# Optimization experiments

Hardware: AMD Instinct MI355X
Metric: run time of the kernel (lower is better)

The kernel has to match this reference:

```python
import jax, jax.numpy as jnp
import numpy as np

N_CLUSTERS = 256
EMBED_DIM = 128
ALPHA = 1.0


def setup_inputs() -> dict:
    key = jax.random.key(0)
    k1, k2 = jax.random.split(key)
    inputs = jax.random.normal(k1, (200000, EMBED_DIM), dtype=jnp.float32)
    clusters = jax.random.normal(k2, (N_CLUSTERS, EMBED_DIM), dtype=jnp.float32)
    return {"inputs": inputs, "clusters": clusters}


def reference(inputs, clusters):
    # Squared euclidean distance via the GEMM trick instead of an [N, K, D]
    x_sq = jnp.sum(inputs * inputs, axis=1, keepdims=True)          # [N, 1]
    c_sq = jnp.sum(clusters * clusters, axis=1)[None, :]             # [1, K]
    cross = inputs @ clusters.T                                      # [N, K]
    dist2 = jnp.maximum(x_sq + c_sq - 2.0 * cross, 0.0)              # [N, K]
    q = 1.0 / (1.0 + dist2 / ALPHA)
    q = q ** ((ALPHA + 1.0) / 2.0)
    q = q / jnp.sum(q, axis=1, keepdims=True)
    return q
```

## Files before the change

### kernel.cpp

```cpp
#include <hip/hip_runtime.h>


#define DIM 128
#define NK  256
#define TM  64
#define THREADS 512
#define LSTR 136

typedef __attribute__((ext_vector_type(8))) short short8;
typedef __attribute__((ext_vector_type(4))) float floatx4;

__device__ __forceinline__ unsigned short bf16_rne(float f) {
    unsigned int u = __float_as_uint(f);
    return (unsigned short)((u + 0x7fffu + ((u >> 16) & 1u)) >> 16);
}
__device__ __forceinline__ float bf16_f(unsigned short h) {
    return __uint_as_float(((unsigned int)h) << 16);
}

__global__ __launch_bounds__(THREADS, 4) void cluster_q_mfma(
    const float* __restrict__ x,
    const float* __restrict__ c,
    float* __restrict__ out)
{
    __shared__ __align__(16) unsigned short xs_hi[TM][LSTR];
    __shared__ __align__(16) unsigned short xs_lo[TM][LSTR];
    __shared__ float xsq_s[TM];
    __shared__ float psum[TM][8];
    __shared__ float inv_s[TM];

    const int tid  = threadIdx.x;
    const int wave = tid >> 6;
    const int lane = tid & 63;
    const int lm   = lane & 15;
    const int q4   = lane >> 4;
    const size_t row0 = (size_t)blockIdx.x * TM;

    {
        const int r  = tid >> 3;
        const int cb = (tid & 7) * 16;
        const float4* xg = (const float4*)(x + (row0 + r) * DIM + cb);
        float4 f4[4];
        #pragma unroll
        for (int i = 0; i < 4; ++i) f4[i] = xg[i];
        const float* fv = (const float*)f4;
        union { unsigned short u[16]; short8 v[2]; } H, L;
        float s = 0.f;
        #pragma unroll
        for (int i = 0; i < 16; ++i) {
            float f = fv[i];
            s = fmaf(f, f, s);
            unsigned short h = bf16_rne(f);
            H.u[i] = h;
            L.u[i] = bf16_rne(f - bf16_f(h));
        }
        *(short8*)&xs_hi[r][cb]     = H.v[0];
        *(short8*)&xs_hi[r][cb + 8] = H.v[1];
        *(short8*)&xs_lo[r][cb]     = L.v[0];
        *(short8*)&xs_lo[r][cb + 8] = L.v[1];
        s += __shfl_xor(s, 1);
        s += __shfl_xor(s, 2);
        s += __shfl_xor(s, 4);
        if ((tid & 7) == 0) xsq_s[r] = s;
    }

    short8 bf[2][4];
    float csq[2];
    #pragma unroll
    for (int ct = 0; ct < 2; ++ct) {
        float cp = 0.f;
        const int col = wave * 32 + ct * 16 + lm;
        #pragma unroll
        for (int ks = 0; ks < 4; ++ks) {
            const float4* cg = (const float4*)(c + col * DIM + ks * 32 + q4 * 8);
            float4 b0 = cg[0], b1 = cg[1];
            const float* bv0 = (const float*)&b0;
            const float* bv1 = (const float*)&b1;
            union { unsigned short u[8]; short8 v; } B;
            #pragma unroll
            for (int i = 0; i < 4; ++i) {
                float f = bv0[i];
                cp = fmaf(f, f, cp);
                B.u[i] = bf16_rne(f);
            }
            #pragma unroll
            for (int i = 0; i < 4; ++i) {
                float f = bv1[i];
                cp = fmaf(f, f, cp);
                B.u[4 + i] = bf16_rne(f);
            }
            bf[ct][ks] = B.v;
        }
        cp += __shfl_xor(cp, 16);
        cp += __shfl_xor(cp, 32);
        csq[ct] = cp;
    }

    floatx4 acc[4][2];
    #pragma unroll
    for (int rt = 0; rt < 4; ++rt)
        #pragma unroll
        for (int ct = 0; ct < 2; ++ct)
            acc[rt][ct] = (floatx4){0.f, 0.f, 0.f, 0.f};

    __syncthreads();

    #pragma unroll
    for (int ks = 0; ks < 4; ++ks) {
        const int ko = ks * 32 + q4 * 8;
        #pragma unroll
        for (int rt = 0; rt < 4; ++rt) {
            short8 ah = *(const short8*)&xs_hi[rt * 16 + lm][ko];
            short8 al = *(const short8*)&xs_lo[rt * 16 + lm][ko];
            #pragma unroll
            for (int ct = 0; ct < 2; ++ct) {
                acc[rt][ct] = __builtin_amdgcn_mfma_f32_16x16x32_bf16(ah, bf[ct][ks], acc[rt][ct], 0, 0, 0);
                acc[rt][ct] = __builtin_amdgcn_mfma_f32_16x16x32_bf16(al, bf[ct][ks], acc[rt][ct], 0, 0, 0);
            }
        }
    }

    #pragma unroll
    for (int rt = 0; rt < 4; ++rt) {
        #pragma unroll
        for (int reg = 0; reg < 4; ++reg) {
            const int r = rt * 16 + q4 * 4 + reg;
            const float xq = xsq_s[r];
            float p = 0.f;
            #pragma unroll
            for (int ct = 0; ct < 2; ++ct) {
                float d2 = xq + csq[ct] - 2.f * acc[rt][ct][reg];
                d2 = fmaxf(d2, 0.f);
                float q = 1.f / (1.f + d2);
                acc[rt][ct][reg] = q;
                p += q;
            }
            p += __shfl_xor(p, 1);
            p += __shfl_xor(p, 2);
            p += __shfl_xor(p, 4);
            p += __shfl_xor(p, 8);
            if (lm == 0) psum[r][wave] = p;
        }
    }
    __syncthreads();

    if (tid < TM) {
        float s = 0.f;
        #pragma unroll
        for (int w = 0; w < 8; ++w) s += psum[tid][w];
        inv_s[tid] = 1.f / s;
    }
    __syncthreads();

    #pragma unroll
    for (int rt = 0; rt < 4; ++rt) {
        #pragma unroll
        for (int reg = 0; reg < 4; ++reg) {
            const int r = rt * 16 + q4 * 4 + reg;
            const float inv = inv_s[r];
            #pragma unroll
            for (int ct = 0; ct < 2; ++ct) {
                out[(row0 + r) * NK + wave * 32 + ct * 16 + lm] = acc[rt][ct][reg] * inv;
            }
        }
    }
}

extern "C" void kernel_launch(void* const* d_in, const int* in_sizes, int n_in,
                              void* d_out, int out_size, void* d_ws, size_t ws_size,
                              hipStream_t stream) {
    const float* x = (const float*)d_in[0];
    const float* c = (const float*)d_in[1];
    float* out = (float*)d_out;
    int N = in_sizes[0] / DIM;
    cluster_q_mfma<<<dim3(N / TM), dim3(THREADS), 0, stream>>>(x, c, out);
}
```

Before: 329.1 us.

## Precompute bf16 clusters in prep kernel and give each wave full rows

Adds a small prep kernel that converts the cluster matrix to bf16 in MFMA fragment order and computes cluster squared norms into workspace, so the main kernel stops redoing that work in every block. The main kernel now uses 256 threads, with each wave owning 16 rows across all 256 clusters and loading x straight into registers. This removes the x LDS staging, the cross-wave partial-sum exchange and two barriers. It also uses fast reciprocal intrinsics. The cost is a second launch, reading B fragments from global/L2 in each block, and more accumulator registers per thread.

```diff
diff --git a/kernel.cpp b/kernel.cpp
--- a/kernel.cpp
+++ b/kernel.cpp
@@ -3,9 +3,6 @@
 
 #define DIM 128
 #define NK  256
-#define TM  64
-#define THREADS 512
-#define LSTR 136
 
 typedef __attribute__((ext_vector_type(8))) short short8;
 typedef __attribute__((ext_vector_type(4))) float floatx4;
@@ -18,151 +15,141 @@
     return __uint_as_float(((unsigned int)h) << 16);
 }
 
-__global__ __launch_bounds__(THREADS, 4) void cluster_q_mfma(
+__global__ void prep_clusters(const float* __restrict__ c,
+                              unsigned short* __restrict__ wb,
+                              float* __restrict__ wcsq)
+{
+    if (blockIdx.x < 8) {
+        const int gid  = blockIdx.x * 512 + threadIdx.x;
+        const int lane = gid & 63;
+        const int ks   = (gid >> 6) & 3;
+        const int ct   = gid >> 8;
+        const int lm   = lane & 15;
+        const int q4   = lane >> 4;
+        const int col  = ct * 16 + lm;
+        const float4* cg = (const float4*)(c + col * DIM + ks * 32 + q4 * 8);
+        float4 v0 = cg[0], v1 = cg[1];
+        const float* f0 = (const float*)&v0;
+        const float* f1 = (const float*)&v1;
+        union { unsigned short u[8]; short8 v; } B;
+        #pragma unroll
+        for (int i = 0; i < 4; ++i) B.u[i] = bf16_rne(f0[i]);
+        #pragma unroll
+        for (int i = 0; i < 4; ++i) B.u[4 + i] = bf16_rne(f1[i]);
+        ((short8*)wb)[gid] = B.v;
+    } else {
+        const int t = threadIdx.x;
+        const int col = t >> 1, half = t & 1;
+        const float4* cg = (const float4*)(c + col * DIM + half * 64);
+        float s = 0.f;
+        #pragma unroll
+        for (int i = 0; i < 16; ++i) {
+            float4 v = cg[i];
+            s = fmaf(v.x, v.x, s); s = fmaf(v.y, v.y, s);
+            s = fmaf(v.z, v.z, s); s = fmaf(v.w, v.w, s);
+        }
+        s += __shfl_xor(s, 1);
+        if (!half) wcsq[col] = s;
+    }
+}
+
+__global__ __launch_bounds__(256, 3) void cluster_q_v2(
     const float* __restrict__ x,
-    const float* __restrict__ c,
+    const unsigned short* __restrict__ wb,
+    const float* __restrict__ wcsq,
     float* __restrict__ out)
 {
-    __shared__ __align__(16) unsigned short xs_hi[TM][LSTR];
-    __shared__ __align__(16) unsigned short xs_lo[TM][LSTR];
-    __shared__ float xsq_s[TM];
-    __shared__ float psum[TM][8];
-    __shared__ float inv_s[TM];
+    __shared__ float csq_s[NK];
+    const int tid  = threadIdx.x;
+    csq_s[tid] = wcsq[tid];
 
-    const int tid  = threadIdx.x;
     const int wave = tid >> 6;
     const int lane = tid & 63;
     const int lm   = lane & 15;
     const int q4   = lane >> 4;
-    const size_t row0 = (size_t)blockIdx.x * TM;
+    const size_t row0 = (size_t)blockIdx.x * 64 + wave * 16;
 
-    {
-        const int r  = tid >> 3;
-        const int cb = (tid & 7) * 16;
-        const float4* xg = (const float4*)(x + (row0 + r) * DIM + cb);
-        float4 f4[4];
+    short8 ah[4], al[4];
+    float xq = 0.f;
+    const float* xrow = x + (row0 + lm) * DIM;
+    #pragma unroll
+    for (int ks = 0; ks < 4; ++ks) {
+        const float4* xg = (const float4*)(xrow + ks * 32 + q4 * 8);
+        float4 v0 = xg[0], v1 = xg[1];
+        const float* f0 = (const float*)&v0;
+        const float* f1 = (const float*)&v1;
+        union { unsigned short u[8]; short8 v; } H, L;
         #pragma unroll
-        for (int i = 0; i < 4; ++i) f4[i] = xg[i];
-        const float* fv = (const float*)f4;
-        union { unsigned short u[16]; short8 v[2]; } H, L;
-        float s = 0.f;
-        #pragma unroll
-        for (int i = 0; i < 16; ++i) {
-            float f = fv[i];
-            s = fmaf(f, f, s);
+        for (int i = 0; i < 4; ++i) {
+            float f = f0[i];
+            xq = fmaf(f, f, xq);
             unsigned short h = bf16_rne(f);
             H.u[i] = h;
             L.u[i] = bf16_rne(f - bf16_f(h));
         }
-        *(short8*)&xs_hi[r][cb]     = H.v[0];
-        *(short8*)&xs_hi[r][cb + 8] = H.v[1];
-        *(short8*)&xs_lo[r][cb]     = L.v[0];
-        *(short8*)&xs_lo[r][cb + 8] = L.v[1];
-        s += __shfl_xor(s, 1);
-        s += __shfl_xor(s, 2);
-        s += __shfl_xor(s, 4);
-        if ((tid & 7) == 0) xsq_s[r] = s;
+        #pragma unroll
+        for (int i = 0; i < 4; ++i) {
+            float f = f1[i];
+            xq = fmaf(f, f, xq);
+            unsigned short h = bf16_rne(f);
+            H.u[4 + i] = h;
+            L.u[4 + i] = bf16_rne(f - bf16_f(h));
+        }
+        ah[ks] = H.v;
+        al[ks] = L.v;
     }
+    xq += __shfl_xor(xq, 16);
+    xq += __shfl_xor(xq, 32);
 
-    short8 bf[2][4];
-    float csq[2];
+    floatx4 acc[16];
     #pragma unroll
-    for (int ct = 0; ct < 2; ++ct) {
-        float cp = 0.f;
-        const int col = wave * 32 + ct * 16 + lm;
+    for (int ct = 0; ct < 16; ++ct) {
+        const short8* bp = (const short8*)wb + (ct * 256 + lane);
+        floatx4 a = (floatx4){0.f, 0.f, 0.f, 0.f};
         #pragma unroll
         for (int ks = 0; ks < 4; ++ks) {
-            const float4* cg = (const float4*)(c + col * DIM + ks * 32 + q4 * 8);
-            float4 b0 = cg[0], b1 = cg[1];
-            const float* bv0 = (const float*)&b0;
-            const float* bv1 = (const float*)&b1;
-            union { unsigned short u[8]; short8 v; } B;
-            #pragma unroll
-            for (int i = 0; i < 4; ++i) {
-                float f = bv0[i];
-                cp = fmaf(f, f, cp);
-                B.u[i] = bf16_rne(f);
-            }
-            #pragma unroll
-            for (int i = 0; i < 4; ++i) {
-                float f = bv1[i];
-                cp = fmaf(f, f, cp);
-                B.u[4 + i] = bf16_rne(f);
-            }
-            bf[ct][ks] = B.v;
+            short8 b = bp[ks * 64];
+            a = __builtin_amdgcn_mfma_f32_16x16x32_bf16(ah[ks], b, a, 0, 0, 0);
+            a = __builtin_amdgcn_mfma_f32_16x16x32_bf16(al[ks], b, a, 0, 0, 0);
         }
-        cp += __shfl_xor(cp, 16);
-        cp += __shfl_xor(cp, 32);
-        csq[ct] = cp;
+        acc[ct] = a;
     }
-
-    floatx4 acc[4][2];
-    #pragma unroll
-    for (int rt = 0; rt < 4; ++rt)
-        #pragma unroll
-        for (int ct = 0; ct < 2; ++ct)
-            acc[rt][ct] = (floatx4){0.f, 0.f, 0.f, 0.f};
 
     __syncthreads();
 
+    float xs4[4];
     #pragma unroll
-    for (int ks = 0; ks < 4; ++ks) {
-        const int ko = ks * 32 + q4 * 8;
+    for (int r = 0; r < 4; ++r) xs4[r] = __shfl(xq, q4 * 4 + r);
+
+    float rsum[4] = {0.f, 0.f, 0.f, 0.f};
+    #pragma unroll
+    for (int ct = 0; ct < 16; ++ct) {
+        const float cq = csq_s[ct * 16 + lm];
         #pragma unroll
-        for (int rt = 0; rt < 4; ++rt) {
-            short8 ah = *(const short8*)&xs_hi[rt * 16 + lm][ko];
-            short8 al = *(const short8*)&xs_lo[rt * 16 + lm][ko];
-            #pragma unroll
-            for (int ct = 0; ct < 2; ++ct) {
-                acc[rt][ct] = __builtin_amdgcn_mfma_f32_16x16x32_bf16(ah, bf[ct][ks], acc[rt][ct], 0, 0, 0);
-                acc[rt][ct] = __builtin_amdgcn_mfma_f32_16x16x32_bf16(al, bf[ct][ks], acc[rt][ct], 0, 0, 0);
-            }
+        for (int r = 0; r < 4; ++r) {
+            float d2 = fmaf(-2.f, acc[ct][r], xs4[r] + cq);
+            d2 = fmaxf(d2, 0.f);
+            float q = __builtin_amdgcn_rcpf(1.f + d2);
+            acc[ct][r] = q;
+            rsum[r] += q;
         }
+    }
+    #pragma unroll
+    for (int r = 0; r < 4; ++r) {
+        rsum[r] += __shfl_xor(rsum[r], 1);
+        rsum[r] += __shfl_xor(rsum[r], 2);
+        rsum[r] += __shfl_xor(rsum[r], 4);
+        rsum[r] += __shfl_xor(rsum[r], 8);
+        rsum[r] = __builtin_amdgcn_rcpf(rsum[r]);
     }
 
     #pragma unroll
-    for (int rt = 0; rt < 4; ++rt) {
+    for (int r = 0; r < 4; ++r) {
+        float* op = out + (row0 + q4 * 4 + r) * NK + lm;
+        const float inv = rsum[r];
         #pragma unroll
-        for (int reg = 0; reg < 4; ++reg) {
-            const int r = rt * 16 + q4 * 4 + reg;
-            const float xq = xsq_s[r];
-            float p = 0.f;
-            #pragma unroll
-            for (int ct = 0; ct < 2; ++ct) {
-                float d2 = xq + csq[ct] - 2.f * acc[rt][ct][reg];
-                d2 = fmaxf(d2, 0.f);
-                float q = 1.f / (1.f + d2);
-                acc[rt][ct][reg] = q;
-                p += q;
-            }
-            p += __shfl_xor(p, 1);
-            p += __shfl_xor(p, 2);
-            p += __shfl_xor(p, 4);
-            p += __shfl_xor(p, 8);
-            if (lm == 0) psum[r][wave] = p;
-        }
-    }
-    __syncthreads();
-
-    if (tid < TM) {
-        float s = 0.f;
-        #pragma unroll
-        for (int w = 0; w < 8; ++w) s += psum[tid][w];
-        inv_s[tid] = 1.f / s;
-    }
-    __syncthreads();
-
-    #pragma unroll
-    for (int rt = 0; rt < 4; ++rt) {
-        #pragma unroll
-        for (int reg = 0; reg < 4; ++reg) {
-            const int r = rt * 16 + q4 * 4 + reg;
-            const float inv = inv_s[r];
-            #pragma unroll
-            for (int ct = 0; ct < 2; ++ct) {
-                out[(row0 + r) * NK + wave * 32 + ct * 16 + lm] = acc[rt][ct][reg] * inv;
-            }
-        }
+        for (int ct = 0; ct < 16; ++ct)
+            op[ct * 16] = acc[ct][r] * inv;
     }
 }
 
@@ -172,6 +159,10 @@
     const float* x = (const float*)d_in[0];
     const float* c = (const float*)d_in[1];
     float* out = (float*)d_out;
-    int N = in_sizes[0] / DIM;
-    cluster_q_mfma<<<dim3(N / TM), dim3(THREADS), 0, stream>>>(x, c, out);
+    unsigned short* wb = (unsigned short*)d_ws;
+    float* wcsq = (float*)((char*)d_ws + 65536);
+    const int N = in_sizes[0] / DIM;
+
+    prep_clusters<<<dim3(9), dim3(512), 0, stream>>>(c, wb, wcsq);
+    cluster_q_v2<<<dim3(N / 64), dim3(256), 0, stream>>>(x, wb, wcsq, out);
 }
```

Result: slower. 348.0 us (+5.7%).
